# Kernel tuning notes

Measured on AMD Instinct MI355X. Metric: run time of the kernel, lower is better.

The kernel has to match this reference:

```python
import jax, jax.numpy as jnp
import numpy as np

BS, S, D, H, HS, HSEL, L = 32, 512, 512, 8, 2, 4, 6
DK = D // H  # 64
HD = H - HS  # dynamic heads


def setup_inputs() -> dict:
    key = jax.random.key(0)
    ks = jax.random.split(key, 10)
    w = lambda k, shape: jax.random.normal(k, shape, dtype=jnp.float32) * 0.02
    return {
        'q_embed_data': jax.random.normal(ks[0], (BS, S, D), jnp.float32),
        'qa_embed_data': jax.random.normal(ks[1], (BS, S, D), jnp.float32),
        # stacked per-layer params (torch Linear convention: W[out,in], y = x@W.T+b)
        'Wq': w(ks[2], (L, D, D)), 'bq': jnp.zeros((L, D), jnp.float32),
        'Wv': w(ks[3], (L, D, D)), 'bv': jnp.zeros((L, D), jnp.float32),
        'Wg': w(ks[4], (L, HD, D)),                      # routing gate, no bias
        'Wo': w(ks[5], (L, D, D)), 'bo': jnp.zeros((L, D), jnp.float32),
        'ln1_g': jnp.ones((L, D), jnp.float32), 'ln1_b': jnp.zeros((L, D), jnp.float32),
        'W1': w(ks[6], (L, D, D)), 'b1': jnp.zeros((L, D), jnp.float32),
        'W2': w(ks[7], (L, D, D)), 'b2': jnp.zeros((L, D), jnp.float32),
        'ln2_g': jnp.ones((L, D), jnp.float32), 'ln2_b': jnp.zeros((L, D), jnp.float32),
    }


def _layer_norm(x, g, b):
    m = x.mean(-1, keepdims=True)
    v = ((x - m) ** 2).mean(-1, keepdims=True)
    return (x - m) * jax.lax.rsqrt(v + 1e-5) * g + b


def _moh_attention(xq, xv, Wq, bq, Wv, bv, Wg, Wo, bo, strict):
    bs, s, d = xq.shape
    q = xq @ Wq.T + bq            # kq_same=True: k = q projection
    v = xv @ Wv.T + bv
    qh = q.reshape(bs, s, H, DK).transpose(0, 2, 1, 3)   # [b,h,s,dk]
    vh = v.reshape(bs, s, H, DK).transpose(0, 2, 1, 3)
    scores = jnp.einsum('bhqd,bhkd->bhqk', qh, qh) / jnp.sqrt(jnp.float32(DK))
    # mask==1 -> causal incl. diag; mask==0 -> strictly causal
    allow = jnp.tril(jnp.ones((s, s), bool), k=-1 if strict else 0)
    scores = jnp.where(allow, scores, jnp.float32(-1e9))
    # pad-zero shift: first query row replaced by zeros -> uniform attention
    scores = scores.at[:, :, 0, :].set(0.0)
    # per-token top-k head routing over dynamic heads
    gates = jax.nn.softmax(q.reshape(bs * s, D) @ Wg.T, axis=-1)  # [bs*s, HD]
    _, idx = jax.lax.top_k(gates, HSEL)
    dmask = jnp.zeros_like(gates).at[jnp.arange(bs * s)[:, None], idx].set(1.0)
    dyn = (gates * dmask).reshape(bs, s, HD)
    routing = jnp.concatenate([jnp.ones((bs, s, HS), gates.dtype), dyn], -1).mean(1)  # [b,H]
    attn = jax.nn.softmax(scores, axis=-1)
    ctx = jnp.einsum('bhqk,bhkd->bhqd', attn, vh) * routing[:, :, None, None]
    out = ctx.transpose(0, 2, 1, 3).reshape(bs, s, D) @ Wo.T + bo
    f = dmask.sum(0)
    P = gates.mean(0)
    balance = jnp.sum((f / (f.sum() + 1e-5)) * (P / (P.sum() + 1e-5)))
    return out, balance


def reference(q_embed_data, qa_embed_data, Wq, bq, Wv, bv, Wg, Wo, bo,
              ln1_g, ln1_b, W1, b1, W2, b2, ln2_g, ln2_b):
    def layer(i, xq, xv, strict):
        a, bl = _moh_attention(xq, xv, Wq[i], bq[i], Wv[i], bv[i], Wg[i], Wo[i], bo[i], strict)
        x = _layer_norm(xq + a, ln1_g[i], ln1_b[i])
        ffn = jax.nn.relu(x @ W1[i].T + b1[i]) @ W2[i].T + b2[i]
        return _layer_norm(x + ffn, ln2_g[i], ln2_b[i]), bl

    y = qa_embed_data
    x = q_embed_data
    # blocks_1: self-attention on y, mask=1
    y, _ = layer(0, y, y, False)
    y, _ = layer(1, y, y, False)
    # blocks_2: alternate mask=1 self-attn / mask=0 cross-attn (values=y)
    x, _ = layer(2, x, x, False)
    x, bl = layer(3, x, y, True)
    x, _ = layer(4, x, x, False)
    x, bl = layer(5, x, y, True)
    return (x, bl)
```

## Files before the change

### kernel.cpp

```cpp
#include <hip/hip_runtime.h>
#include <cstdint>

#define BSZ 32
#define SEQ 512
#define DM  512
#define NH  8
#define DK  64
#define HS_ 2
#define HD_ 6
#define NL  6
#define MROWS (BSZ*SEQ)
#define QVLD 1024
#define SCL 0.18033688011112043f

typedef unsigned short bf16_t;
typedef __attribute__((ext_vector_type(4))) float f32x4;
typedef __attribute__((ext_vector_type(8))) short bf16x8;
typedef __attribute__((ext_vector_type(8))) unsigned short u16x8;

#define DEV static __device__ __forceinline__

DEV float bf2f(bf16_t b) {
  unsigned int u = ((unsigned int)b) << 16;
  float f; __builtin_memcpy(&f, &u, 4); return f;
}
DEV bf16_t f2b(float f) {
  unsigned int u; __builtin_memcpy(&u, &f, 4);
  unsigned int r = (u + 0x7fffu + ((u >> 16) & 1u)) >> 16;
  return (bf16_t)r;
}
DEV void unp2(unsigned int w, float& a, float& b) {
  unsigned int ua = w << 16, ub = w & 0xffff0000u;
  __builtin_memcpy(&a, &ua, 4); __builtin_memcpy(&b, &ub, 4);
}
DEV unsigned cvtpk(float lo, float hi) {
  unsigned r;
  asm("v_cvt_pk_bf16_f32 %0, %1, %2" : "=v"(r) : "v"(lo), "v"(hi));
  return r;
}

DEV void gload_lds16(const bf16_t* g, bf16_t* l) {
  __builtin_amdgcn_global_load_lds(
      (const __attribute__((address_space(1))) void*)g,
      (__attribute__((address_space(3))) void*)l, 16, 0, 0);
}

__global__ __launch_bounds__(256) void f2b_kernel(const float* __restrict__ in,
                                                  bf16_t* __restrict__ out, int n4) {
  int i = blockIdx.x * 256 + threadIdx.x;
  int stride = gridDim.x * 256;
  for (; i < n4; i += stride) {
    float4 v = reinterpret_cast<const float4*>(in)[i];
    ushort4 o;
    o.x = f2b(v.x); o.y = f2b(v.y); o.z = f2b(v.z); o.w = f2b(v.w);
    reinterpret_cast<ushort4*>(out)[i] = o;
  }
}

__global__ __launch_bounds__(256) void f2bw_kernel(
    const float* __restrict__ s0, const float* __restrict__ s1,
    const float* __restrict__ s2, const float* __restrict__ s3,
    const float* __restrict__ s4, bf16_t* __restrict__ dst) {
  const float* srcs[5] = {s0, s1, s2, s3, s4};
  const float* s = srcs[blockIdx.y];
  bf16_t* d = dst + (size_t)blockIdx.y * ((size_t)NL * DM * DM);
  const int i = blockIdx.x * 256 + threadIdx.x;
  float4 v = reinterpret_cast<const float4*>(s)[i];
  ushort4 o;
  o.x = f2b(v.x); o.y = f2b(v.y); o.z = f2b(v.z); o.w = f2b(v.w);
  reinterpret_cast<ushort4*>(d)[i] = o;
}

__global__ __launch_bounds__(256) void gemm_qv(
    const bf16_t* __restrict__ A0, const bf16_t* __restrict__ A1,
    const bf16_t* __restrict__ W0, const bf16_t* __restrict__ W1,
    const float* __restrict__ b0, const float* __restrict__ b1,
    bf16_t* __restrict__ Yb) {
  const int K = 512;
  const int lin = blockIdx.y * 8 + blockIdx.x;
  const int swz = (lin & 7) * 128 + (lin >> 3);
  const int bn = swz & 7, bm = swz >> 3;
  const int tid = threadIdx.x, wid = tid >> 6, lane = tid & 63;
  const int wr = wid >> 1, wc = wid & 1;
  __shared__ __align__(16) bf16_t As[128 * 64];
  __shared__ __align__(16) bf16_t Bs[128 * 64];

  const bool hi = bn >= 4;
  const bf16_t* Asel = hi ? A1 : A0;
  const bf16_t* Wsel = hi ? (W1 - (size_t)512 * K) : W0;
  const float* bsel = hi ? (b1 - 512) : b0;

  f32x4 acc[4][4];
#pragma unroll
  for (int m = 0; m < 4; ++m)
#pragma unroll
    for (int n = 0; n < 4; ++n) acc[m][n] = f32x4{0.f, 0.f, 0.f, 0.f};

  const int lrow = lane & 15, lko = (lane >> 4) * 8;
  const int sr = wid * 8 + (lane >> 3), scol = (lane & 7) * 8;
  const size_t arow0 = (size_t)bm * 128, brow0 = (size_t)bn * 128;

  for (int k0 = 0; k0 < K; k0 += 64) {
#pragma unroll
    for (int i = 0; i < 4; ++i) {
      gload_lds16(Asel + (arow0 + i * 32 + sr) * K + k0 + scol, &As[(i * 4 + wid) * 512]);
      gload_lds16(Wsel + (brow0 + i * 32 + sr) * K + k0 + scol, &Bs[(i * 4 + wid) * 512]);
    }
    __syncthreads();
    bf16x8 af[4][2], bw[4][2];
#pragma unroll
    for (int m = 0; m < 4; ++m)
#pragma unroll
      for (int ks = 0; ks < 2; ++ks)
        af[m][ks] = *reinterpret_cast<const bf16x8*>(
            &As[(wr * 64 + m * 16 + lrow) * 64 + ks * 32 + lko]);
#pragma unroll
    for (int n = 0; n < 4; ++n)
#pragma unroll
      for (int ks = 0; ks < 2; ++ks)
        bw[n][ks] = *reinterpret_cast<const bf16x8*>(
            &Bs[(wc * 64 + n * 16 + lrow) * 64 + ks * 32 + lko]);
    __builtin_amdgcn_s_setprio(1);
#pragma unroll
    for (int ks = 0; ks < 2; ++ks)
#pragma unroll
      for (int m = 0; m < 4; ++m)
#pragma unroll
        for (int n = 0; n < 4; ++n)
          acc[m][n] = __builtin_amdgcn_mfma_f32_16x16x32_bf16(af[m][ks], bw[n][ks], acc[m][n], 0, 0, 0);
    __builtin_amdgcn_s_setprio(0);
    __syncthreads();
  }

  const int r0 = bm * 128 + wr * 64 + (lane >> 4) * 4;
  const int c0 = bn * 128 + wc * 64 + lrow;
#pragma unroll
  for (int n = 0; n < 4; ++n) {
    const int col = c0 + n * 16;
    const float bc = bsel[col];
#pragma unroll
    for (int m = 0; m < 4; ++m)
#pragma unroll
      for (int j = 0; j < 4; ++j)
        Yb[(size_t)(r0 + m * 16 + j) * QVLD + col] = f2b(acc[m][n][j] + bc);
  }
}

template <bool RELU>
__global__ __launch_bounds__(256) void gemm_n512(
    const bf16_t* __restrict__ A, const bf16_t* __restrict__ W,
    const float* __restrict__ bias, bf16_t* __restrict__ Yb) {
  const int K = 512;
  const int lin = blockIdx.y * 4 + blockIdx.x;
  const int swz = (lin & 7) * 128 + (lin >> 3);
  const int bn = swz & 3, bm = swz >> 2;
  const int tid = threadIdx.x, wid = tid >> 6, lane = tid & 63;
  const int wr = wid >> 1, wc = wid & 1;
  __shared__ __align__(16) bf16_t As[64 * 64];
  __shared__ __align__(16) bf16_t Bs[128 * 64];

  f32x4 acc[2][4];
#pragma unroll
  for (int m = 0; m < 2; ++m)
#pragma unroll
    for (int n = 0; n < 4; ++n) acc[m][n] = f32x4{0.f, 0.f, 0.f, 0.f};

  const int lrow = lane & 15, lko = (lane >> 4) * 8;
  const int sr = wid * 8 + (lane >> 3), scol = (lane & 7) * 8;
  const size_t arow0 = (size_t)bm * 64, brow0 = (size_t)bn * 128;

  for (int k0 = 0; k0 < K; k0 += 64) {
#pragma unroll
    for (int i = 0; i < 2; ++i)
      gload_lds16(A + (arow0 + i * 32 + sr) * K + k0 + scol, &As[(i * 4 + wid) * 512]);
#pragma unroll
    for (int i = 0; i < 4; ++i)
      gload_lds16(W + (brow0 + i * 32 + sr) * K + k0 + scol, &Bs[(i * 4 + wid) * 512]);
    __syncthreads();
    bf16x8 af[2][2], bw[4][2];
#pragma unroll
    for (int m = 0; m < 2; ++m)
#pragma unroll
      for (int ks = 0; ks < 2; ++ks)
        af[m][ks] = *reinterpret_cast<const bf16x8*>(
            &As[(wr * 32 + m * 16 + lrow) * 64 + ks * 32 + lko]);
#pragma unroll
    for (int n = 0; n < 4; ++n)
#pragma unroll
      for (int ks = 0; ks < 2; ++ks)
        bw[n][ks] = *reinterpret_cast<const bf16x8*>(
            &Bs[(wc * 64 + n * 16 + lrow) * 64 + ks * 32 + lko]);
    __builtin_amdgcn_s_setprio(1);
#pragma unroll
    for (int ks = 0; ks < 2; ++ks)
#pragma unroll
      for (int m = 0; m < 2; ++m)
#pragma unroll
        for (int n = 0; n < 4; ++n)
          acc[m][n] = __builtin_amdgcn_mfma_f32_16x16x32_bf16(af[m][ks], bw[n][ks], acc[m][n], 0, 0, 0);
    __builtin_amdgcn_s_setprio(0);
    __syncthreads();
  }

  const int r0 = bm * 64 + wr * 32 + (lane >> 4) * 4;
  const int c0 = bn * 128 + wc * 64 + lrow;
#pragma unroll
  for (int n = 0; n < 4; ++n) {
    const int col = c0 + n * 16;
    const float bc = bias[col];
#pragma unroll
    for (int m = 0; m < 2; ++m)
#pragma unroll
      for (int j = 0; j < 4; ++j) {
        float v = acc[m][n][j] + bc;
        if (RELU) v = fmaxf(v, 0.f);
        Yb[(size_t)(r0 + m * 16 + j) * DM + col] = f2b(v);
      }
  }
}

__global__ __launch_bounds__(256) void gates_kernel(
    const bf16_t* __restrict__ qv, const float* __restrict__ Wg,
    float* __restrict__ rdyn, float* __restrict__ fP) {
  __shared__ float wg_s[HD_ * DM];
  __shared__ float blk[4][18];
  const int tid = threadIdx.x, wid = tid >> 6, lane = tid & 63;
  for (int i = tid; i < HD_ * DM / 4; i += 256)
    reinterpret_cast<float4*>(wg_s)[i] = reinterpret_cast<const float4*>(Wg)[i];
  __syncthreads();
  const int bb = blockIdx.x >> 3;
  const int t0 = (blockIdx.x & 7) * 64 + wid * 16;
  float fs[6] = {0, 0, 0, 0, 0, 0}, ps[6] = {0, 0, 0, 0, 0, 0}, rs[6] = {0, 0, 0, 0, 0, 0};
  for (int it = 0; it < 16; ++it) {
    const int tok = bb * SEQ + t0 + it;
    uint4 u = reinterpret_cast<const uint4*>(qv + (size_t)tok * QVLD)[lane];
    float x[8];
    unp2(u.x, x[0], x[1]); unp2(u.y, x[2], x[3]);
    unp2(u.z, x[4], x[5]); unp2(u.w, x[6], x[7]);
    float g[6];
#pragma unroll
    for (int j = 0; j < 6; ++j) {
      float p = 0.f;
#pragma unroll
      for (int e = 0; e < 8; ++e) p = fmaf(x[e], wg_s[j * DM + lane * 8 + e], p);
#pragma unroll
      for (int off = 32; off; off >>= 1) p += __shfl_xor(p, off);
      g[j] = p;
    }
    float mx = g[0];
#pragma unroll
    for (int j = 1; j < 6; ++j) mx = fmaxf(mx, g[j]);
    float se = 0.f;
#pragma unroll
    for (int j = 0; j < 6; ++j) { g[j] = __expf(g[j] - mx); se += g[j]; }
    float inv = 1.f / se;
#pragma unroll
    for (int j = 0; j < 6; ++j) g[j] *= inv;
    int d1 = 0;
#pragma unroll
    for (int j = 1; j < 6; ++j)
      if (g[j] < g[d1] || (g[j] == g[d1] && j > d1)) d1 = j;
    int d2 = (d1 == 0) ? 1 : 0;
#pragma unroll
    for (int j = 0; j < 6; ++j) {
      if (j == d1) continue;
      if (g[j] < g[d2] || (g[j] == g[d2] && j > d2)) d2 = j;
    }
#pragma unroll
    for (int j = 0; j < 6; ++j) {
      const bool drop = (j == d1) || (j == d2);
      fs[j] += drop ? 0.f : 1.f;
      ps[j] += g[j];
      rs[j] += drop ? 0.f : g[j];
    }
  }
  if (lane == 0) {
#pragma unroll
    for (int j = 0; j < 6; ++j) {
      blk[wid][j] = fs[j]; blk[wid][6 + j] = ps[j]; blk[wid][12 + j] = rs[j];
    }
  }
  __syncthreads();
  if (tid < 18) {
    float s = blk[0][tid] + blk[1][tid] + blk[2][tid] + blk[3][tid];
    if (tid < 12) atomicAdd(&fP[tid], s);
    else atomicAdd(&rdyn[bb * 6 + (tid - 12)], s * (1.f / 512.f));
  }
}

__global__ __launch_bounds__(256) void rowzero_kernel(
    const bf16_t* __restrict__ qv, const float* __restrict__ rdyn,
    bf16_t* __restrict__ ctx) {
  const int h = blockIdx.x, b = blockIdx.y;
  const int tid = threadIdx.x;
  const int c8 = tid & 7;
  const int rc = tid >> 3;
  const bf16_t* vb = qv + 512 + ((size_t)(b * SEQ)) * QVLD + h * DK + c8 * 8;
  float s[8] = {0, 0, 0, 0, 0, 0, 0, 0};
  for (int i = 0; i < 16; ++i) {
    u16x8 vv = *reinterpret_cast<const u16x8*>(vb + (size_t)(rc * 16 + i) * QVLD);
#pragma unroll
    for (int e = 0; e < 8; ++e) s[e] += bf2f(vv[e]);
  }
  __shared__ float red[64][33];
#pragma unroll
  for (int e = 0; e < 8; ++e) red[c8 * 8 + e][rc] = s[e];
  __syncthreads();
  if (tid < 64) {
    float t = 0.f;
#pragma unroll
    for (int c = 0; c < 32; ++c) t += red[tid][c];
    const float factor = (h < HS_) ? 1.f : rdyn[b * 6 + (h - HS_)];
    ctx[((size_t)(b * SEQ)) * DM + h * DK + tid] = f2b(t * (1.f / 512.f) * factor);
  }
}

__global__ __launch_bounds__(256, 2) void fattn_kernel(
    const bf16_t* __restrict__ qv, const float* __restrict__ rdyn,
    bf16_t* __restrict__ ctx, int strict) {
  const int lin = (blockIdx.z * 8 + blockIdx.y) * 2 + blockIdx.x;
  const int swz = (lin & 7) * 64 + (lin >> 3);
  const int bx = swz & 1, h = (swz >> 1) & 7, b = swz >> 4;
  const int tid = threadIdx.x, wid = tid >> 6, lane = tid & 63;
  const int c0 = lane & 15, grp = lane >> 4;
  const int l3 = lane >> 3, c3 = lane & 7;
  const int kidx = lane & 31, dhalf = lane >> 5;

  __shared__ __align__(16) bf16_t Ks[64 * 64];
  __shared__ __align__(16) bf16_t Vt[64 * 72];
  __shared__ __align__(16) bf16_t Ps[4][32 * 64];

  const bf16_t* qp = qv;
  const bf16_t* vp = qv + 512;
  const float factor = (h < HS_) ? 1.f : rdyn[b * 6 + (h - HS_)];

  const int qtA = bx, qtB = 3 - bx;
  const int qbaseA = qtA * 128 + wid * 32;
  const int qbaseB = qtB * 128 + wid * 32;

  bf16x8 qfA[2][2], qfB[2][2];
#pragma unroll
  for (int nt = 0; nt < 2; ++nt)
#pragma unroll
    for (int ks = 0; ks < 2; ++ks) {
      qfA[nt][ks] = *reinterpret_cast<const bf16x8*>(
          qp + ((size_t)(b * SEQ + qbaseA + nt * 16 + c0)) * QVLD + h * DK + ks * 32 + grp * 8);
      qfB[nt][ks] = *reinterpret_cast<const bf16x8*>(
          qp + ((size_t)(b * SEQ + qbaseB + nt * 16 + c0)) * QVLD + h * DK + ks * 32 + grp * 8);
    }

  f32x4 accA[2][4], accB[2][4];
#pragma unroll
  for (int m = 0; m < 2; ++m)
#pragma unroll
    for (int d = 0; d < 4; ++d) {
      accA[m][d] = f32x4{0.f, 0.f, 0.f, 0.f};
      accB[m][d] = f32x4{0.f, 0.f, 0.f, 0.f};
    }
  float mA[2] = {-3e38f, -3e38f}, lA[2] = {0.f, 0.f};
  float mB[2] = {-3e38f, -3e38f}, lB[2] = {0.f, 0.f};

  const int lastA = (qbaseA + 31 - strict) >> 6;
  const int lastB = (qbaseB + 31 - strict) >> 6;
  const int ktmax = 2 * qtB + 1;

  auto do_tile = [&](bf16x8 (&qf)[2][2], f32x4 (&acc)[2][4], float (&mreg)[2],
                     float (&lreg)[2], int qbase, bool masked, int kt) {
    const char* KsB = (const char*)Ks;
    bf16x8 kf[4][2];
#pragma unroll
    for (int mt = 0; mt < 4; ++mt)
#pragma unroll
      for (int ks = 0; ks < 2; ++ks)
        kf[mt][ks] = *reinterpret_cast<const bf16x8*>(
            KsB + (mt * 16 + c0) * 128 + 16 * ((4 * ks + grp) ^ (c0 & 7)));
    f32x4 s[4][2];
#pragma unroll
    for (int mt = 0; mt < 4; ++mt)
#pragma unroll
      for (int nt = 0; nt < 2; ++nt) s[mt][nt] = f32x4{0.f, 0.f, 0.f, 0.f};
    __builtin_amdgcn_s_setprio(1);
#pragma unroll
    for (int mt = 0; mt < 4; ++mt)
#pragma unroll
      for (int nt = 0; nt < 2; ++nt)
#pragma unroll
        for (int ks = 0; ks < 2; ++ks)
          s[mt][nt] = __builtin_amdgcn_mfma_f32_16x16x32_bf16(
              kf[mt][ks], qf[nt][ks], s[mt][nt], 0, 0, 0);
    __builtin_amdgcn_s_setprio(0);

    float sc[2];
#pragma unroll
    for (int nt = 0; nt < 2; ++nt) {
      const int q = qbase + nt * 16 + c0;
#pragma unroll
      for (int mt = 0; mt < 4; ++mt)
#pragma unroll
        for (int j = 0; j < 4; ++j) {
          int k = kt * 64 + mt * 16 + grp * 4 + j;
          float t = s[mt][nt][j] * SCL;
          if (masked && (k + strict > q)) t = -1e30f;
          s[mt][nt][j] = t;
        }
      float mx = -3e38f;
#pragma unroll
      for (int mt = 0; mt < 4; ++mt)
#pragma unroll
        for (int j = 0; j < 4; ++j) mx = fmaxf(mx, s[mt][nt][j]);
      mx = fmaxf(mx, __shfl_xor(mx, 16));
      mx = fmaxf(mx, __shfl_xor(mx, 32));
      const float mnew = fmaxf(mreg[nt], mx);
      sc[nt] = exp2f(mreg[nt] - mnew);
      mreg[nt] = mnew;
      float ts = 0.f;
#pragma unroll
      for (int mt = 0; mt < 4; ++mt)
#pragma unroll
        for (int j = 0; j < 4; ++j) {
          float pp = exp2f(s[mt][nt][j] - mnew);
          s[mt][nt][j] = pp; ts += pp;
        }
      ts += __shfl_xor(ts, 16);
      ts += __shfl_xor(ts, 32);
      lreg[nt] = lreg[nt] * sc[nt] + ts;
    }
    char* PsB = (char*)(&Ps[wid][0]);
#pragma unroll
    for (int nt = 0; nt < 2; ++nt)
#pragma unroll
      for (int mt = 0; mt < 4; ++mt) {
        uint2 w;
        w.x = cvtpk(s[mt][nt][0], s[mt][nt][1]);
        w.y = cvtpk(s[mt][nt][2], s[mt][nt][3]);
        int row = nt * 16 + c0;
        int off = (row * 128 + mt * 32 + grp * 8) ^ ((c0 & 7) << 4);
        *reinterpret_cast<uint2*>(PsB + off) = w;
      }
#pragma unroll
    for (int mtq = 0; mtq < 2; ++mtq) {
      f32x4 sv;
#pragma unroll
      for (int j = 0; j < 4; ++j) sv[j] = __shfl(sc[mtq], grp * 4 + j);
#pragma unroll
      for (int dt = 0; dt < 4; ++dt) acc[mtq][dt] *= sv;
    }
    bf16x8 pf[2][2], vf2[4][2];
#pragma unroll
    for (int mtq = 0; mtq < 2; ++mtq)
#pragma unroll
      for (int ks = 0; ks < 2; ++ks)
        pf[mtq][ks] = *reinterpret_cast<const bf16x8*>(
            PsB + (mtq * 16 + c0) * 128 + 16 * ((4 * ks + grp) ^ (c0 & 7)));
#pragma unroll
    for (int dt = 0; dt < 4; ++dt)
#pragma unroll
      for (int ks = 0; ks < 2; ++ks)
        vf2[dt][ks] = *reinterpret_cast<const bf16x8*>(
            (const char*)Vt + (dt * 16 + c0) * 144 + ks * 64 + grp * 16);
    __builtin_amdgcn_s_setprio(1);
#pragma unroll
    for (int mtq = 0; mtq < 2; ++mtq)
#pragma unroll
      for (int dt = 0; dt < 4; ++dt)
#pragma unroll
        for (int ks = 0; ks < 2; ++ks)
          acc[mtq][dt] = __builtin_amdgcn_mfma_f32_16x16x32_bf16(
              pf[mtq][ks], vf2[dt][ks], acc[mtq][dt], 0, 0, 0);
    __builtin_amdgcn_s_setprio(0);
  };

  for (int kt = 0; kt <= ktmax; ++kt) {
#pragma unroll
    for (int i = 0; i < 2; ++i) {
      int row = i * 32 + wid * 8 + l3;
      int blk = c3 ^ l3;
      gload_lds16(qp + ((size_t)(b * SEQ + kt * 64 + row)) * QVLD + h * DK + blk * 8,
                  Ks + (i * 32 + wid * 8) * 64);
    }
#pragma unroll
    for (int j = 0; j < 2; ++j) {
      const int p = wid * 2 + j;
      const int d0 = p * 8 + dhalf * 4;
      const bf16_t* src = vp + ((size_t)(b * SEQ + kt * 64 + 2 * kidx)) * QVLD + h * DK + d0;
      ushort4 lo = *reinterpret_cast<const ushort4*>(src);
      ushort4 hv = *reinterpret_cast<const ushort4*>(src + QVLD);
      *reinterpret_cast<unsigned*>(&Vt[(d0 + 0) * 72 + 2 * kidx]) = (unsigned)lo.x | ((unsigned)hv.x << 16);
      *reinterpret_cast<unsigned*>(&Vt[(d0 + 1) * 72 + 2 * kidx]) = (unsigned)lo.y | ((unsigned)hv.y << 16);
      *reinterpret_cast<unsigned*>(&Vt[(d0 + 2) * 72 + 2 * kidx]) = (unsigned)lo.z | ((unsigned)hv.z << 16);
      *reinterpret_cast<unsigned*>(&Vt[(d0 + 3) * 72 + 2 * kidx]) = (unsigned)lo.w | ((unsigned)hv.w << 16);
    }
    __syncthreads();
    if (kt <= lastB) do_tile(qfB, accB, mB, lB, qbaseB, kt == lastB, kt);
    if (kt <= lastA) do_tile(qfA, accA, mA, lA, qbaseA, kt == lastA, kt);
    __syncthreads();
  }

#pragma unroll
  for (int e = 0; e < 2; ++e) {
    const int qbase = e ? qbaseB : qbaseA;
    f32x4 (&acc)[2][4] = e ? accB : accA;
    float (&lreg)[2] = e ? lB : lA;
#pragma unroll
    for (int mtq = 0; mtq < 2; ++mtq) {
      const float inv = factor / lreg[mtq];
      f32x4 iv;
#pragma unroll
      for (int j = 0; j < 4; ++j) iv[j] = __shfl(inv, grp * 4 + j);
#pragma unroll
      for (int j = 0; j < 4; ++j) {
        const int q = qbase + mtq * 16 + grp * 4 + j;
        if (q == 0) continue;
#pragma unroll
        for (int dt = 0; dt < 4; ++dt)
          ctx[((size_t)(b * SEQ + q)) * DM + h * DK + dt * 16 + c0] =
              f2b(acc[mtq][dt][j] * iv[j]);
      }
    }
  }
}

template <int OUT>
__global__ __launch_bounds__(256) void add_ln_kernel(
    const bf16_t* __restrict__ X, const bf16_t* __restrict__ A2,
    const float* __restrict__ gam, const float* __restrict__ bet,
    bf16_t* __restrict__ outb, float* __restrict__ outf) {
  const int wid = threadIdx.x >> 6, lane = threadIdx.x & 63;
  const size_t row = (size_t)blockIdx.x * 4 + wid;
  const size_t base = row * DM + lane * 8;
  uint4 xu = *reinterpret_cast<const uint4*>(X + base);
  uint4 au = *reinterpret_cast<const uint4*>(A2 + base);
  float z[8];
  {
    float p0, p1, q0, q1;
    unp2(xu.x, p0, p1); unp2(au.x, q0, q1); z[0] = p0 + q0; z[1] = p1 + q1;
    unp2(xu.y, p0, p1); unp2(au.y, q0, q1); z[2] = p0 + q0; z[3] = p1 + q1;
    unp2(xu.z, p0, p1); unp2(au.z, q0, q1); z[4] = p0 + q0; z[5] = p1 + q1;
    unp2(xu.w, p0, p1); unp2(au.w, q0, q1); z[6] = p0 + q0; z[7] = p1 + q1;
  }
  float s = 0.f;
#pragma unroll
  for (int e = 0; e < 8; ++e) s += z[e];
#pragma unroll
  for (int off = 32; off; off >>= 1) s += __shfl_xor(s, off);
  const float mean = s * (1.f / 512.f);
  float ss = 0.f;
#pragma unroll
  for (int e = 0; e < 8; ++e) { float d = z[e] - mean; ss += d * d; }
#pragma unroll
  for (int off = 32; off; off >>= 1) ss += __shfl_xor(ss, off);
  const float inv = rsqrtf(ss * (1.f / 512.f) + 1e-5f);
  float4 g0 = *reinterpret_cast<const float4*>(gam + lane * 8);
  float4 g1 = *reinterpret_cast<const float4*>(gam + lane * 8 + 4);
  float4 b0 = *reinterpret_cast<const float4*>(bet + lane * 8);
  float4 b1 = *reinterpret_cast<const float4*>(bet + lane * 8 + 4);
  float o[8];
  o[0] = (z[0] - mean) * inv * g0.x + b0.x;
  o[1] = (z[1] - mean) * inv * g0.y + b0.y;
  o[2] = (z[2] - mean) * inv * g0.z + b0.z;
  o[3] = (z[3] - mean) * inv * g0.w + b0.w;
  o[4] = (z[4] - mean) * inv * g1.x + b1.x;
  o[5] = (z[5] - mean) * inv * g1.y + b1.y;
  o[6] = (z[6] - mean) * inv * g1.z + b1.z;
  o[7] = (z[7] - mean) * inv * g1.w + b1.w;
  if (OUT == 0) {
    uint4 w;
    w.x = (unsigned)f2b(o[0]) | ((unsigned)f2b(o[1]) << 16);
    w.y = (unsigned)f2b(o[2]) | ((unsigned)f2b(o[3]) << 16);
    w.z = (unsigned)f2b(o[4]) | ((unsigned)f2b(o[5]) << 16);
    w.w = (unsigned)f2b(o[6]) | ((unsigned)f2b(o[7]) << 16);
    *reinterpret_cast<uint4*>(outb + base) = w;
  } else {
    float4 f0, f1;
    f0.x = o[0]; f0.y = o[1]; f0.z = o[2]; f0.w = o[3];
    f1.x = o[4]; f1.y = o[5]; f1.z = o[6]; f1.w = o[7];
    *reinterpret_cast<float4*>(outf + base) = f0;
    *reinterpret_cast<float4*>(outf + base + 4) = f1;
  }
}

__global__ void balance_kernel(const float* __restrict__ fP, float* __restrict__ out) {
  if (threadIdx.x == 0 && blockIdx.x == 0) {
    float fs = 0.f, pssum = 0.f, P[6];
    for (int j = 0; j < 6; ++j) {
      fs += fP[j];
      P[j] = fP[6 + j] * (1.f / (float)MROWS);
      pssum += P[j];
    }
    float bal = 0.f;
    for (int j = 0; j < 6; ++j)
      bal += (fP[j] / (fs + 1e-5f)) * (P[j] / (pssum + 1e-5f));
    out[0] = bal;
  }
}

extern "C" void kernel_launch(void* const* d_in, const int* in_sizes, int n_in,
                              void* d_out, int out_size, void* d_ws, size_t ws_size,
                              hipStream_t stream) {
  (void)in_sizes; (void)n_in; (void)out_size; (void)ws_size;
  const float* q_embed  = (const float*)d_in[0];
  const float* qa_embed = (const float*)d_in[1];
  const float* Wq  = (const float*)d_in[2];
  const float* bq  = (const float*)d_in[3];
  const float* Wv  = (const float*)d_in[4];
  const float* bv  = (const float*)d_in[5];
  const float* Wg  = (const float*)d_in[6];
  const float* Wo  = (const float*)d_in[7];
  const float* bo  = (const float*)d_in[8];
  const float* ln1g = (const float*)d_in[9];
  const float* ln1b = (const float*)d_in[10];
  const float* W1  = (const float*)d_in[11];
  const float* b1  = (const float*)d_in[12];
  const float* W2  = (const float*)d_in[13];
  const float* b2  = (const float*)d_in[14];
  const float* ln2g = (const float*)d_in[15];
  const float* ln2b = (const float*)d_in[16];

  char* p = (char*)d_ws;
  auto alloc = [&](size_t bytes) -> char* {
    char* r = p; p += (bytes + 255) & ~(size_t)255; return r;
  };
  const size_t WDE = (size_t)NL * DM * DM;
  const size_t AE  = (size_t)MROWS * DM;
  bf16_t* wall_b = (bf16_t*)alloc(5 * WDE * 2);
  bf16_t* wq_b = wall_b;
  bf16_t* wv_b = wall_b + WDE;
  bf16_t* wo_b = wall_b + 2 * WDE;
  bf16_t* w1_b = wall_b + 3 * WDE;
  bf16_t* w2_b = wall_b + 4 * WDE;
  bf16_t* y_b   = (bf16_t*)alloc(AE * 2);
  bf16_t* x_b   = (bf16_t*)alloc(AE * 2);
  bf16_t* qv_b  = (bf16_t*)alloc((size_t)MROWS * QVLD * 2);
  bf16_t* ctx_b = (bf16_t*)alloc(AE * 2);
  bf16_t* x1_b  = (bf16_t*)alloc(AE * 2);
  bf16_t* tmp_b = (bf16_t*)alloc(AE * 2);
  bf16_t* ffn1_b = (bf16_t*)alloc(AE * 2);
  float* rdyn = (float*)alloc(BSZ * 6 * 4);
  float* fP   = (float*)alloc(NL * 12 * 4);

  hipMemsetAsync(fP, 0, NL * 12 * 4, stream);

  f2bw_kernel<<<dim3((unsigned)(WDE / 4 / 256), 5), 256, 0, stream>>>(
      Wq, Wv, Wo, W1, W2, wall_b);
  f2b_kernel<<<2048, 256, 0, stream>>>(qa_embed, y_b, (int)(AE / 4));
  f2b_kernel<<<2048, 256, 0, stream>>>(q_embed, x_b, (int)(AE / 4));

  const size_t DD = (size_t)DM * DM;
  dim3 gqv(8, 128), gn5(4, 256);
  float* outx = (float*)d_out;

  auto layer = [&](int i, bf16_t* resb, const bf16_t* xvb, int strict, bool last) {
    hipMemsetAsync(rdyn, 0, BSZ * 6 * 4, stream);
    gemm_qv<<<gqv, 256, 0, stream>>>(
        resb, xvb, wq_b + i * DD, wv_b + i * DD, bq + i * DM, bv + i * DM, qv_b);
    gates_kernel<<<MROWS / 64, 256, 0, stream>>>(qv_b, Wg + (size_t)i * HD_ * DM, rdyn, fP + i * 12);
    rowzero_kernel<<<dim3(NH, BSZ), 256, 0, stream>>>(qv_b, rdyn, ctx_b);
    fattn_kernel<<<dim3(2, NH, BSZ), 256, 0, stream>>>(qv_b, rdyn, ctx_b, strict);
    gemm_n512<false><<<gn5, 256, 0, stream>>>(ctx_b, wo_b + i * DD, bo + i * DM, tmp_b);
    add_ln_kernel<0><<<MROWS / 4, 256, 0, stream>>>(
        resb, tmp_b, ln1g + i * DM, ln1b + i * DM, x1_b, nullptr);
    gemm_n512<true><<<gn5, 256, 0, stream>>>(x1_b, w1_b + i * DD, b1 + i * DM, ffn1_b);
    gemm_n512<false><<<gn5, 256, 0, stream>>>(ffn1_b, w2_b + i * DD, b2 + i * DM, tmp_b);
    if (last)
      add_ln_kernel<1><<<MROWS / 4, 256, 0, stream>>>(
          x1_b, tmp_b, ln2g + i * DM, ln2b + i * DM, nullptr, outx);
    else
      add_ln_kernel<0><<<MROWS / 4, 256, 0, stream>>>(
          x1_b, tmp_b, ln2g + i * DM, ln2b + i * DM, resb, nullptr);
  };

  layer(0, y_b, y_b, 0, false);
  layer(1, y_b, y_b, 0, false);
  layer(2, x_b, x_b, 0, false);
  layer(3, x_b, y_b, 1, false);
  layer(4, x_b, x_b, 0, false);
  layer(5, x_b, y_b, 1, true);
  balance_kernel<<<1, 64, 0, stream>>>(fP + 5 * 12, outx + (size_t)MROWS * DM);
}
```

Baseline: 1.050 ms.

## Double-buffer K/V tiles in flash attention and fuse row-zero mean into it

The attention kernel now double-buffers the K and V shared-memory tiles, prefetching the next tile while computing on the current one, which drops one barrier per iteration. The separate row-zero kernel is removed: blocks with bx==0 (which sweep every key tile) accumulate V column sums while transposing V and write the uniform-attention row for query 0. Per-layer memsets are replaced by a single memset over per-layer stat slices, and the two activation conversions merge into one launch. This raises shared memory use and register pressure in the attention kernel, which may hurt occupancy at two blocks per CU.

```diff
diff --git a/kernel.cpp b/kernel.cpp
--- a/kernel.cpp
+++ b/kernel.cpp
@@ -45,16 +45,16 @@
       (__attribute__((address_space(3))) void*)l, 16, 0, 0);
 }
 
-__global__ __launch_bounds__(256) void f2b_kernel(const float* __restrict__ in,
-                                                  bf16_t* __restrict__ out, int n4) {
-  int i = blockIdx.x * 256 + threadIdx.x;
-  int stride = gridDim.x * 256;
-  for (; i < n4; i += stride) {
-    float4 v = reinterpret_cast<const float4*>(in)[i];
-    ushort4 o;
-    o.x = f2b(v.x); o.y = f2b(v.y); o.z = f2b(v.z); o.w = f2b(v.w);
-    reinterpret_cast<ushort4*>(out)[i] = o;
-  }
+__global__ __launch_bounds__(256) void f2b2_kernel(
+    const float* __restrict__ s0, const float* __restrict__ s1,
+    bf16_t* __restrict__ d0, bf16_t* __restrict__ d1) {
+  const float* s = blockIdx.y ? s1 : s0;
+  bf16_t* d = blockIdx.y ? d1 : d0;
+  const int i = blockIdx.x * 256 + threadIdx.x;
+  float4 v = reinterpret_cast<const float4*>(s)[i];
+  ushort4 o;
+  o.x = f2b(v.x); o.y = f2b(v.y); o.z = f2b(v.z); o.w = f2b(v.w);
+  reinterpret_cast<ushort4*>(d)[i] = o;
 }
 
 __global__ __launch_bounds__(256) void f2bw_kernel(
@@ -288,33 +288,6 @@
   }
 }
 
-__global__ __launch_bounds__(256) void rowzero_kernel(
-    const bf16_t* __restrict__ qv, const float* __restrict__ rdyn,
-    bf16_t* __restrict__ ctx) {
-  const int h = blockIdx.x, b = blockIdx.y;
-  const int tid = threadIdx.x;
-  const int c8 = tid & 7;
-  const int rc = tid >> 3;
-  const bf16_t* vb = qv + 512 + ((size_t)(b * SEQ)) * QVLD + h * DK + c8 * 8;
-  float s[8] = {0, 0, 0, 0, 0, 0, 0, 0};
-  for (int i = 0; i < 16; ++i) {
-    u16x8 vv = *reinterpret_cast<const u16x8*>(vb + (size_t)(rc * 16 + i) * QVLD);
-#pragma unroll
-    for (int e = 0; e < 8; ++e) s[e] += bf2f(vv[e]);
-  }
-  __shared__ float red[64][33];
-#pragma unroll
-  for (int e = 0; e < 8; ++e) red[c8 * 8 + e][rc] = s[e];
-  __syncthreads();
-  if (tid < 64) {
-    float t = 0.f;
-#pragma unroll
-    for (int c = 0; c < 32; ++c) t += red[tid][c];
-    const float factor = (h < HS_) ? 1.f : rdyn[b * 6 + (h - HS_)];
-    ctx[((size_t)(b * SEQ)) * DM + h * DK + tid] = f2b(t * (1.f / 512.f) * factor);
-  }
-}
-
 __global__ __launch_bounds__(256, 2) void fattn_kernel(
     const bf16_t* __restrict__ qv, const float* __restrict__ rdyn,
     bf16_t* __restrict__ ctx, int strict) {
@@ -326,9 +299,10 @@
   const int l3 = lane >> 3, c3 = lane & 7;
   const int kidx = lane & 31, dhalf = lane >> 5;
 
-  __shared__ __align__(16) bf16_t Ks[64 * 64];
-  __shared__ __align__(16) bf16_t Vt[64 * 72];
+  __shared__ __align__(16) bf16_t Ks[2][64 * 64];
+  __shared__ __align__(16) bf16_t Vt[2][64 * 72];
   __shared__ __align__(16) bf16_t Ps[4][32 * 64];
+  __shared__ float csum[64];
 
   const bf16_t* qp = qv;
   const bf16_t* vp = qv + 512;
@@ -359,14 +333,51 @@
     }
   float mA[2] = {-3e38f, -3e38f}, lA[2] = {0.f, 0.f};
   float mB[2] = {-3e38f, -3e38f}, lB[2] = {0.f, 0.f};
+  float cs[8] = {0, 0, 0, 0, 0, 0, 0, 0};
 
   const int lastA = (qbaseA + 31 - strict) >> 6;
   const int lastB = (qbaseB + 31 - strict) >> 6;
   const int ktmax = 2 * qtB + 1;
 
+  auto stageK = [&](int kt, bf16_t* dst) {
+#pragma unroll
+    for (int i = 0; i < 2; ++i) {
+      int row = i * 32 + wid * 8 + l3;
+      int blk = c3 ^ l3;
+      gload_lds16(qp + ((size_t)(b * SEQ + kt * 64 + row)) * QVLD + h * DK + blk * 8,
+                  dst + (i * 32 + wid * 8) * 64);
+    }
+  };
+  auto loadV = [&](int kt, ushort4 (&lo)[2], ushort4 (&hv)[2]) {
+#pragma unroll
+    for (int j = 0; j < 2; ++j) {
+      const int d0 = (wid * 2 + j) * 8 + dhalf * 4;
+      const bf16_t* src = vp + ((size_t)(b * SEQ + kt * 64 + 2 * kidx)) * QVLD + h * DK + d0;
+      lo[j] = *reinterpret_cast<const ushort4*>(src);
+      hv[j] = *reinterpret_cast<const ushort4*>(src + QVLD);
+    }
+  };
+  auto writeV = [&](bf16_t* Vtb, ushort4 (&lo)[2], ushort4 (&hv)[2]) {
+#pragma unroll
+    for (int j = 0; j < 2; ++j) {
+      const int d0 = (wid * 2 + j) * 8 + dhalf * 4;
+      *reinterpret_cast<unsigned*>(&Vtb[(d0 + 0) * 72 + 2 * kidx]) = (unsigned)lo[j].x | ((unsigned)hv[j].x << 16);
+      *reinterpret_cast<unsigned*>(&Vtb[(d0 + 1) * 72 + 2 * kidx]) = (unsigned)lo[j].y | ((unsigned)hv[j].y << 16);
+      *reinterpret_cast<unsigned*>(&Vtb[(d0 + 2) * 72 + 2 * kidx]) = (unsigned)lo[j].z | ((unsigned)hv[j].z << 16);
+      *reinterpret_cast<unsigned*>(&Vtb[(d0 + 3) * 72 + 2 * kidx]) = (unsigned)lo[j].w | ((unsigned)hv[j].w << 16);
+      if (bx == 0) {
+        cs[j * 4 + 0] += bf2f(lo[j].x) + bf2f(hv[j].x);
+        cs[j * 4 + 1] += bf2f(lo[j].y) + bf2f(hv[j].y);
+        cs[j * 4 + 2] += bf2f(lo[j].z) + bf2f(hv[j].z);
+        cs[j * 4 + 3] += bf2f(lo[j].w) + bf2f(hv[j].w);
+      }
+    }
+  };
+
   auto do_tile = [&](bf16x8 (&qf)[2][2], f32x4 (&acc)[2][4], float (&mreg)[2],
-                     float (&lreg)[2], int qbase, bool masked, int kt) {
-    const char* KsB = (const char*)Ks;
+                     float (&lreg)[2], int qbase, bool masked, int kt,
+                     const bf16_t* Ksb, const bf16_t* Vtb) {
+    const char* KsB = (const char*)Ksb;
     bf16x8 kf[4][2];
 #pragma unroll
     for (int mt = 0; mt < 4; ++mt)
@@ -457,7 +468,7 @@
 #pragma unroll
       for (int ks = 0; ks < 2; ++ks)
         vf2[dt][ks] = *reinterpret_cast<const bf16x8*>(
-            (const char*)Vt + (dt * 16 + c0) * 144 + ks * 64 + grp * 16);
+            (const char*)Vtb + (dt * 16 + c0) * 144 + ks * 64 + grp * 16);
     __builtin_amdgcn_s_setprio(1);
 #pragma unroll
     for (int mtq = 0; mtq < 2; ++mtq)
@@ -470,31 +481,42 @@
     __builtin_amdgcn_s_setprio(0);
   };
 
-  for (int kt = 0; kt <= ktmax; ++kt) {
-#pragma unroll
-    for (int i = 0; i < 2; ++i) {
-      int row = i * 32 + wid * 8 + l3;
-      int blk = c3 ^ l3;
-      gload_lds16(qp + ((size_t)(b * SEQ + kt * 64 + row)) * QVLD + h * DK + blk * 8,
-                  Ks + (i * 32 + wid * 8) * 64);
-    }
-#pragma unroll
-    for (int j = 0; j < 2; ++j) {
-      const int p = wid * 2 + j;
-      const int d0 = p * 8 + dhalf * 4;
-      const bf16_t* src = vp + ((size_t)(b * SEQ + kt * 64 + 2 * kidx)) * QVLD + h * DK + d0;
-      ushort4 lo = *reinterpret_cast<const ushort4*>(src);
-      ushort4 hv = *reinterpret_cast<const ushort4*>(src + QVLD);
-      *reinterpret_cast<unsigned*>(&Vt[(d0 + 0) * 72 + 2 * kidx]) = (unsigned)lo.x | ((unsigned)hv.x << 16);
-      *reinterpret_cast<unsigned*>(&Vt[(d0 + 1) * 72 + 2 * kidx]) = (unsigned)lo.y | ((unsigned)hv.y << 16);
-      *reinterpret_cast<unsigned*>(&Vt[(d0 + 2) * 72 + 2 * kidx]) = (unsigned)lo.z | ((unsigned)hv.z << 16);
-      *reinterpret_cast<unsigned*>(&Vt[(d0 + 3) * 72 + 2 * kidx]) = (unsigned)lo.w | ((unsigned)hv.w << 16);
-    }
+  {
+    ushort4 lo[2], hv[2];
+    stageK(0, Ks[0]);
+    loadV(0, lo, hv);
+    writeV(Vt[0], lo, hv);
     __syncthreads();
-    if (kt <= lastB) do_tile(qfB, accB, mB, lB, qbaseB, kt == lastB, kt);
-    if (kt <= lastA) do_tile(qfA, accA, mA, lA, qbaseA, kt == lastA, kt);
+  }
+
+  int cbuf = 0;
+  for (int kt = 0; kt <= ktmax; ++kt, cbuf ^= 1) {
+    ushort4 lo[2], hv[2];
+    const bool pref = kt < ktmax;
+    if (pref) {
+      stageK(kt + 1, Ks[cbuf ^ 1]);
+      loadV(kt + 1, lo, hv);
+    }
+    if (kt <= lastB) do_tile(qfB, accB, mB, lB, qbaseB, kt == lastB, kt, Ks[cbuf], Vt[cbuf]);
+    if (kt <= lastA) do_tile(qfA, accA, mA, lA, qbaseA, kt == lastA, kt, Ks[cbuf], Vt[cbuf]);
+    if (pref) writeV(Vt[cbuf ^ 1], lo, hv);
     __syncthreads();
   }
+
+  if (bx == 0) {
+#pragma unroll
+    for (int e = 0; e < 8; ++e)
+#pragma unroll
+      for (int off = 1; off <= 16; off <<= 1) cs[e] += __shfl_xor(cs[e], off);
+    if ((lane & 31) == 0) {
+#pragma unroll
+      for (int e = 0; e < 8; ++e)
+        csum[(wid * 2 + (e >> 2)) * 8 + dhalf * 4 + (e & 3)] = cs[e];
+    }
+  }
+  __syncthreads();
+  if (bx == 0 && tid < 64)
+    ctx[((size_t)(b * SEQ)) * DM + h * DK + tid] = f2b(csum[tid] * (1.f / 512.f) * factor);
 
 #pragma unroll
   for (int e = 0; e < 2; ++e) {
@@ -635,26 +657,27 @@
   bf16_t* x1_b  = (bf16_t*)alloc(AE * 2);
   bf16_t* tmp_b = (bf16_t*)alloc(AE * 2);
   bf16_t* ffn1_b = (bf16_t*)alloc(AE * 2);
-  float* rdyn = (float*)alloc(BSZ * 6 * 4);
-  float* fP   = (float*)alloc(NL * 12 * 4);
-
-  hipMemsetAsync(fP, 0, NL * 12 * 4, stream);
+  float* stats = (float*)alloc(NL * (12 + BSZ * 6) * 4);
+  float* fPbase = stats;
+  float* rdynbase = stats + NL * 12;
+
+  hipMemsetAsync(stats, 0, NL * (12 + BSZ * 6) * 4, stream);
 
   f2bw_kernel<<<dim3((unsigned)(WDE / 4 / 256), 5), 256, 0, stream>>>(
       Wq, Wv, Wo, W1, W2, wall_b);
-  f2b_kernel<<<2048, 256, 0, stream>>>(qa_embed, y_b, (int)(AE / 4));
-  f2b_kernel<<<2048, 256, 0, stream>>>(q_embed, x_b, (int)(AE / 4));
+  f2b2_kernel<<<dim3((unsigned)(AE / 4 / 256), 2), 256, 0, stream>>>(
+      qa_embed, q_embed, y_b, x_b);
 
   const size_t DD = (size_t)DM * DM;
   dim3 gqv(8, 128), gn5(4, 256);
   float* outx = (float*)d_out;
 
   auto layer = [&](int i, bf16_t* resb, const bf16_t* xvb, int strict, bool last) {
-    hipMemsetAsync(rdyn, 0, BSZ * 6 * 4, stream);
+    float* fP = fPbase + i * 12;
+    float* rdyn = rdynbase + i * (BSZ * 6);
     gemm_qv<<<gqv, 256, 0, stream>>>(
         resb, xvb, wq_b + i * DD, wv_b + i * DD, bq + i * DM, bv + i * DM, qv_b);
-    gates_kernel<<<MROWS / 64, 256, 0, stream>>>(qv_b, Wg + (size_t)i * HD_ * DM, rdyn, fP + i * 12);
-    rowzero_kernel<<<dim3(NH, BSZ), 256, 0, stream>>>(qv_b, rdyn, ctx_b);
+    gates_kernel<<<MROWS / 64, 256, 0, stream>>>(qv_b, Wg + (size_t)i * HD_ * DM, rdyn, fP);
     fattn_kernel<<<dim3(2, NH, BSZ), 256, 0, stream>>>(qv_b, rdyn, ctx_b, strict);
     gemm_n512<false><<<gn5, 256, 0, stream>>>(ctx_b, wo_b + i * DD, bo + i * DM, tmp_b);
     add_ln_kernel<0><<<MROWS / 4, 256, 0, stream>>>(
@@ -675,5 +698,5 @@
   layer(3, x_b, y_b, 1, false);
   layer(4, x_b, x_b, 0, false);
   layer(5, x_b, y_b, 1, true);
-  balance_kernel<<<1, 64, 0, stream>>>(fP + 5 * 12, outx + (size_t)MROWS * DM);
-}
+  balance_kernel<<<1, 64, 0, stream>>>(fPbase + 5 * 12, outx + (size_t)MROWS * DM);
+}
```

Measured after the change: 1.024 ms. -2.5%, faster.
